# Kernel optimization log

Measured on AMD Instinct MI355X. Metric: run time of the kernel, lower is better.

## Reference

```python
import jax, jax.numpy as jnp
import numpy as np

B, S = 1, 2048
D, HD, NH, NKV, L, V, FF = 2048, 256, 8, 4, 4, 32000, 8192
WINDOW = 1024
SOFTCAP = 50.0
FINAL_CAP = 30.0
EPS = 1e-6
THETA = 10000.0
ATTN_TYPES = ("local", "global", "local", "global")
NEG = -2.3819763e38
SCALE = HD ** -0.5


def _rms(x, w):
    # RMSNorm with unit offset: x * rsqrt(mean(x^2)+eps) * (1 + w)
    n = x * jax.lax.rsqrt(jnp.mean(x * x, axis=-1, keepdims=True) + EPS)
    return n * (1.0 + w)


def _rope(x, cos, sin):
    # x: [B, S, H, HD]; rotate-half formulation (Gemma pairs i with i+HD/2)
    h = HD // 2
    x1, x2 = x[..., :h], x[..., h:]
    c = cos[None, :, None, :]
    s = sin[None, :, None, :]
    return jnp.concatenate([x1 * c - x2 * s, x1 * s + x2 * c], axis=-1)


def setup_inputs() -> dict:
    key = jax.random.key(0)
    ks = jax.random.split(key, 15)
    sd = 0.02
    f = lambda k, shape: jax.random.normal(k, shape, jnp.float32) * sd
    return {
        "input_ids": jax.random.randint(ks[0], (B, S), 0, V),
        "embed": f(ks[1], (V, D)),
        "wq": f(ks[2], (L, NH * HD, D)),
        "wk": f(ks[3], (L, NKV * HD, D)),
        "wv": f(ks[4], (L, NKV * HD, D)),
        "wo": f(ks[5], (L, D, NH * HD)),
        "wg": f(ks[6], (L, FF, D)),
        "wu": f(ks[7], (L, FF, D)),
        "wd": f(ks[8], (L, D, FF)),
        "ln_in": f(ks[9], (L, D)),
        "ln_pa": f(ks[10], (L, D)),
        "ln_pf": f(ks[11], (L, D)),
        "ln_pff": f(ks[12], (L, D)),
        "ln_f": f(ks[13], (D,)),
        "w_lm": f(ks[14], (V, D)),
    }


def _forward(input_ids, embed, wq, wk, wv, wo, wg, wu, wd,
             ln_in, ln_pa, ln_pf, ln_pff, ln_f, w_lm):
    # rotary tables
    pos = jnp.arange(S, dtype=jnp.float32)
    inv = 1.0 / (THETA ** (jnp.arange(0, HD, 2, dtype=jnp.float32) / HD))
    ang = pos[:, None] * inv[None, :]
    cos, sin = jnp.cos(ang), jnp.sin(ang)  # [S, HD/2]

    # additive masks
    i = jnp.arange(S)[:, None]
    j = jnp.arange(S)[None, :]
    causal = jnp.where(j > i, NEG, 0.0).astype(jnp.float32)
    local = jnp.where((j > i) | (i - j >= WINDOW), NEG, 0.0).astype(jnp.float32)

    h = embed[input_ids] * jnp.asarray(D ** 0.5, jnp.float32)
    rep = NH // NKV
    for l in range(L):
        mask = local if ATTN_TYPES[l] == "local" else causal
        x = _rms(h, ln_in[l])
        q = jnp.einsum('bsd,od->bso', x, wq[l]).reshape(B, S, NH, HD)
        k = jnp.einsum('bsd,od->bso', x, wk[l]).reshape(B, S, NKV, HD)
        v = jnp.einsum('bsd,od->bso', x, wv[l]).reshape(B, S, NKV, HD)
        q = _rope(q, cos, sin)
        k = _rope(k, cos, sin)
        k = jnp.repeat(k, rep, axis=2)  # GQA expand
        v = jnp.repeat(v, rep, axis=2)
        q = q.transpose(0, 2, 1, 3)  # bhsd
        k = k.transpose(0, 2, 1, 3)
        v = v.transpose(0, 2, 1, 3)
        qk = jnp.einsum('bhsd,bhfd->bhsf', q, k) * SCALE
        qk = jnp.tanh(qk / SOFTCAP) * SOFTCAP  # attn logit softcap
        scores = jax.nn.softmax(qk + mask, axis=-1)
        a = jnp.einsum('bhsf,bhfd->bhsd', scores, v)
        a = a.transpose(0, 2, 1, 3).reshape(B, S, NH * HD)
        attn_out = jnp.einsum('bso,do->bsd', a, wo[l])
        h = h + _rms(attn_out, ln_pa[l])  # post-attn norm then residual
        x = _rms(h, ln_pf[l])
        gate = jax.nn.gelu(jnp.einsum('bsd,fd->bsf', x, wg[l]), approximate=True)
        up = jnp.einsum('bsd,fd->bsf', x, wu[l])
        mlp = jnp.einsum('bsf,df->bsd', gate * up, wd[l])
        h = h + _rms(mlp, ln_pff[l])
    h = _rms(h, ln_f)
    logits = jnp.einsum('bsd,vd->bsv', h, w_lm)
    return jnp.tanh(logits / FINAL_CAP) * FINAL_CAP


def reference(input_ids, embed, wq, wk, wv, wo, wg, wu, wd,
              ln_in, ln_pa, ln_pf, ln_pff, ln_f, w_lm):
    return _forward(input_ids, embed, wq, wk, wv, wo, wg, wu, wd,
                    ln_in, ln_pa, ln_pf, ln_pff, ln_f, w_lm)
```

## Files before the change

### kernel.cpp

```cpp
#include <hip/hip_runtime.h>
#include <hip/hip_bf16.h>

typedef __attribute__((ext_vector_type(8))) __bf16 bf16x8;
typedef __attribute__((ext_vector_type(4))) float floatx4;

typedef __attribute__((address_space(1))) const unsigned char kGlb;
typedef __attribute__((address_space(3))) unsigned char kLds;

static constexpr int S = 2048;
static constexpr int D = 2048;
static constexpr int HD = 256;
static constexpr int NH = 8;
static constexpr int NKV = 4;
static constexpr int NLAYER = 4;
static constexpr int VOCAB = 32000;
static constexpr int FF = 8192;
static constexpr int WINDOW = 1024;

__device__ __forceinline__ float blk_sum(float v) {
    __shared__ float sm[4];
    #pragma unroll
    for (int o = 32; o > 0; o >>= 1) v += __shfl_down(v, o, 64);
    int lane = threadIdx.x & 63, w = threadIdx.x >> 6;
    __syncthreads();
    if (lane == 0) sm[w] = v;
    __syncthreads();
    return sm[0] + sm[1] + sm[2] + sm[3];
}

__device__ __forceinline__ float blk_max(float v) {
    __shared__ float sm[4];
    #pragma unroll
    for (int o = 32; o > 0; o >>= 1) v = fmaxf(v, __shfl_down(v, o, 64));
    int lane = threadIdx.x & 63, w = threadIdx.x >> 6;
    __syncthreads();
    if (lane == 0) sm[w] = v;
    __syncthreads();
    return fmaxf(fmaxf(sm[0], sm[1]), fmaxf(sm[2], sm[3]));
}

__global__ void embed_kernel(const int* __restrict__ ids, const float* __restrict__ E,
                             float* __restrict__ h) {
    int d = blockIdx.x * 256 + threadIdx.x;
    int s = blockIdx.y;
    h[(long)s * D + d] = E[(long)ids[s] * D + d] * 45.25483399593904f;
}

__global__ void rope_table_kernel(float* __restrict__ c, float* __restrict__ sn) {
    int i = threadIdx.x;
    int p = blockIdx.x;
    float inv = powf(10000.f, -(float)i / 128.f);
    float a = (float)p * inv;
    c[p * 128 + i] = cosf(a);
    sn[p * 128 + i] = sinf(a);
}

__global__ void cvt_bf16_kernel(const float* __restrict__ src, __hip_bfloat16* __restrict__ dst,
                                long n8) {
    long stride = (long)gridDim.x * 256;
    for (long i = (long)blockIdx.x * 256 + threadIdx.x; i < n8; i += stride) {
        long o = i * 8;
        float4 a = *(const float4*)(src + o);
        float4 b = *(const float4*)(src + o + 4);
        __hip_bfloat16 h8[8] = {
            __float2bfloat16(a.x), __float2bfloat16(a.y),
            __float2bfloat16(a.z), __float2bfloat16(a.w),
            __float2bfloat16(b.x), __float2bfloat16(b.y),
            __float2bfloat16(b.z), __float2bfloat16(b.w)};
        *(uint4*)(dst + o) = *(const uint4*)h8;
    }
}

__global__ void rms_bf16_kernel(const float* __restrict__ h, const float* __restrict__ w,
                                __hip_bfloat16* __restrict__ o) {
    int s = blockIdx.x;
    const float* row = h + (long)s * D;
    float vals[8], ss = 0.f;
    #pragma unroll
    for (int t = 0; t < 8; ++t) {
        int j = t * 256 + threadIdx.x;
        float v = row[j]; vals[t] = v; ss += v * v;
    }
    ss = blk_sum(ss);
    float r = rsqrtf(ss * (1.f / D) + 1e-6f);
    #pragma unroll
    for (int t = 0; t < 8; ++t) {
        int j = t * 256 + threadIdx.x;
        o[(long)s * D + j] = __float2bfloat16(vals[t] * r * (1.f + w[j]));
    }
}

__global__ void resid_rms_kernel(float* __restrict__ h, const float* __restrict__ tt,
                                 const float* __restrict__ w) {
    int s = blockIdx.x;
    const float* row = tt + (long)s * D;
    float* hr = h + (long)s * D;
    float vals[8], ss = 0.f;
    #pragma unroll
    for (int t = 0; t < 8; ++t) {
        int j = t * 256 + threadIdx.x;
        float v = row[j]; vals[t] = v; ss += v * v;
    }
    ss = blk_sum(ss);
    float r = rsqrtf(ss * (1.f / D) + 1e-6f);
    #pragma unroll
    for (int t = 0; t < 8; ++t) {
        int j = t * 256 + threadIdx.x;
        hr[j] += vals[t] * r * (1.f + w[j]);
    }
}

__global__ void rope_kernel(__hip_bfloat16* __restrict__ x, const float* __restrict__ cb,
                            const float* __restrict__ sb, int ldx) {
    int s = blockIdx.x, hh = blockIdx.y, i = threadIdx.x;
    __hip_bfloat16* p = x + (long)s * ldx + hh * HD;
    float x1 = __bfloat162float(p[i]);
    float x2 = __bfloat162float(p[128 + i]);
    float c = cb[s * 128 + i], sn = sb[s * 128 + i];
    p[i]       = __float2bfloat16(x1 * c - x2 * sn);
    p[128 + i] = __float2bfloat16(x1 * sn + x2 * c);
}

__global__ void transpose_v_kernel(const __hip_bfloat16* __restrict__ v,
                                   __hip_bfloat16* __restrict__ vt, int ldv) {
    __shared__ ushort tile[64][65];
    int s0 = blockIdx.x * 64, d0 = blockIdx.y * 64, kv = blockIdx.z;
    const ushort* vin = (const ushort*)v;
    ushort* vout = (ushort*)vt;
    #pragma unroll
    for (int it = 0; it < 4; ++it) {
        int slot = it * 256 + threadIdx.x;
        int r = slot >> 4, c4 = (slot & 15) << 2;
        ushort4 x = *(const ushort4*)(vin + (long)(s0 + r) * ldv + kv * HD + d0 + c4);
        tile[r][c4] = x.x; tile[r][c4 + 1] = x.y; tile[r][c4 + 2] = x.z; tile[r][c4 + 3] = x.w;
    }
    __syncthreads();
    #pragma unroll
    for (int it = 0; it < 4; ++it) {
        int slot = it * 256 + threadIdx.x;
        int rr = slot >> 4, c4 = (slot & 15) << 2;
        ushort4 y;
        y.x = tile[c4][rr]; y.y = tile[c4 + 1][rr]; y.z = tile[c4 + 2][rr]; y.w = tile[c4 + 3][rr];
        *(ushort4*)(vout + (long)kv * HD * S + (long)(d0 + rr) * S + s0 + c4) = y;
    }
}

__global__ void softmax_kernel(const float* __restrict__ sc, __hip_bfloat16* __restrict__ pr,
                               int isLocal) {
    int i = blockIdx.x, hh = blockIdx.y;
    const float* row = sc + ((long)hh * S + i) * S;
    __hip_bfloat16* orow = pr + ((long)hh * S + i) * S;
    int lo = isLocal ? max(0, i - (WINDOW - 1)) : 0;
    float vals[8];
    float m = -3.0e38f;
    #pragma unroll
    for (int t = 0; t < 8; ++t) {
        int j = t * 256 + threadIdx.x;
        bool chunkAny = (t * 256 <= i) && (t * 256 + 255 >= lo);
        if (chunkAny) {
            bool valid = (j <= i) && (j >= lo);
            float v = tanhf(row[j] * (0.0625f / 50.f)) * 50.f;
            vals[t] = valid ? v : -3.0e38f;
            m = fmaxf(m, vals[t]);
        } else {
            vals[t] = -3.0e38f;
        }
    }
    m = blk_max(m);
    float ps[8], ssum = 0.f;
    #pragma unroll
    for (int t = 0; t < 8; ++t) {
        float p = (vals[t] > -1.0e38f) ? __expf(vals[t] - m) : 0.f;
        ps[t] = p; ssum += p;
    }
    ssum = blk_sum(ssum);
    float inv = 1.f / ssum;
    #pragma unroll
    for (int t = 0; t < 8; ++t) {
        int j = t * 256 + threadIdx.x;
        orow[j] = __float2bfloat16(ps[t] * inv);
    }
}

__global__ void mul_gu_kernel(__hip_bfloat16* __restrict__ gu) {
    long idx = ((long)blockIdx.x * 256 + threadIdx.x) * 8;
    long s = idx >> 13;
    long f = idx & 8191;
    __hip_bfloat16* gp = gu + s * 16384 + f;
    const __hip_bfloat16* up = gu + s * 16384 + 8192 + f;
    uint4 gv = *(const uint4*)gp;
    uint4 uv = *(const uint4*)up;
    const __hip_bfloat16* gb = (const __hip_bfloat16*)&gv;
    const __hip_bfloat16* ub = (const __hip_bfloat16*)&uv;
    __hip_bfloat16 o[8];
    #pragma unroll
    for (int j = 0; j < 8; ++j)
        o[j] = __float2bfloat16(__bfloat162float(gb[j]) * __bfloat162float(ub[j]));
    *(uint4*)gp = *(const uint4*)o;
}

template<int EPI, int WM, int WN, int MI, int NI>
__global__ __launch_bounds__(WM*WN*64, 2) void gemm_pipe(
    const __hip_bfloat16* __restrict__ A, const __hip_bfloat16* __restrict__ B,
    void* __restrict__ Cv, int K, int lda, int ldb, int ldc,
    long aBatch, long bBatch, long cBatch, int bzDiv, int gx, int kMode) {
    constexpr int T  = WM * WN * 64;
    constexpr int BM = WM * MI * 16;
    constexpr int BN = WN * NI * 16;
    constexpr int AE = BM * 32;
    constexpr int BE = BN * 32;
    __shared__ __hip_bfloat16 lds[4][AE + BE];

    const int tid = threadIdx.x;
    const int nwg = gridDim.x;
    const int orig = blockIdx.x;
    const int wgid = (orig & 7) * (nwg >> 3) + (orig >> 3);
    const int bx = wgid % gx, by = wgid / gx;
    const int bz = blockIdx.z;

    int kstart = 0, kend = K;
    if (kMode == 1) { if (by > bx) return; }
    else if (kMode == 2) { if (by > bx || bx - by >= 9) return; }
    else if (kMode == 3) { kend = min(K, (bx + 1) * BM); }
    else if (kMode == 4) { kend = min(K, (bx + 1) * BM); kstart = max(0, (bx - 1024 / BM) * BM); }

    const __hip_bfloat16* Ab = A + (long)bz * aBatch + (long)bx * BM * lda;
    const __hip_bfloat16* Bb = B + (long)(bz / bzDiv) * bBatch + (long)by * BN * ldb;

    const int w = tid >> 6, l = tid & 63;
    const int wm = w / WN, wn = w % WN;
    const int wrow = wm * MI * 16, wcol = wn * NI * 16;
    const int fr = l & 15, g = l >> 4;
    const int sR = tid >> 2;
    const int sc = tid & 3;

    floatx4 acc[MI][NI] = {};
    bf16x8 bfv[NI];
    bf16x8 af[MI / 2];

    auto stageA = [&](int t, int buf) {
        const int k0 = kstart + t * 32;
        #pragma unroll
        for (int i = 0; i < 2; ++i) {
            int row = sR + i * (T / 4);
            int scol = ((sc ^ ((row >> 1) & 3)) << 3);
            __builtin_amdgcn_global_load_lds(
                (kGlb*)(Ab + (long)row * lda + k0 + scol),
                (kLds*)(&lds[buf][0] + tid * 8 + i * (T * 8)), 16, 0, 0);
        }
    };
    auto stageB = [&](int t, int buf) {
        const int k0 = kstart + t * 32;
        #pragma unroll
        for (int i = 0; i < 2; ++i) {
            int row = sR + i * (T / 4);
            int scol = ((sc ^ ((row >> 1) & 3)) << 3);
            __builtin_amdgcn_global_load_lds(
                (kGlb*)(Bb + (long)row * ldb + k0 + scol),
                (kLds*)(&lds[buf][AE] + tid * 8 + i * (T * 8)), 16, 0, 0);
        }
    };

    auto phase0 = [&](int buf, int t3, bool doStage) {
        const char* AsB = (const char*)&lds[buf][0];
        const char* BsB = (const char*)&lds[buf][AE];
        #pragma unroll
        for (int mi = 0; mi < MI / 2; ++mi) {
            int ra = wrow + mi * 16 + fr;
            af[mi] = *(const bf16x8*)(AsB + ra * 64 + ((g ^ ((ra >> 1) & 3)) << 4));
        }
        #pragma unroll
        for (int ni = 0; ni < NI; ++ni) {
            int rb = wcol + ni * 16 + fr;
            bfv[ni] = *(const bf16x8*)(BsB + rb * 64 + ((g ^ ((rb >> 1) & 3)) << 4));
        }
        if (doStage) stageA(t3, t3 & 3);
        __builtin_amdgcn_s_barrier();
        asm volatile("s_waitcnt lgkmcnt(0)" ::: "memory");
        __builtin_amdgcn_sched_barrier(0);
        __builtin_amdgcn_s_setprio(1);
        #pragma unroll
        for (int mi = 0; mi < MI / 2; ++mi)
            #pragma unroll
            for (int ni = 0; ni < NI; ++ni)
                acc[mi][ni] = __builtin_amdgcn_mfma_f32_16x16x32_bf16(af[mi], bfv[ni], acc[mi][ni], 0, 0, 0);
        __builtin_amdgcn_s_setprio(0);
        __builtin_amdgcn_sched_barrier(0);
        __builtin_amdgcn_s_barrier();
    };

    auto phase1 = [&](int buf, int t3, bool doStage, int vm) {
        const char* AsB = (const char*)&lds[buf][0];
        #pragma unroll
        for (int mi = 0; mi < MI / 2; ++mi) {
            int ra = wrow + (MI / 2 + mi) * 16 + fr;
            af[mi] = *(const bf16x8*)(AsB + ra * 64 + ((g ^ ((ra >> 1) & 3)) << 4));
        }
        if (doStage) stageB(t3, t3 & 3);
        if (vm == 8)      asm volatile("s_waitcnt vmcnt(8)" ::: "memory");
        else if (vm == 4) asm volatile("s_waitcnt vmcnt(4)" ::: "memory");
        else if (vm == 0) asm volatile("s_waitcnt vmcnt(0)" ::: "memory");
        __builtin_amdgcn_s_barrier();
        asm volatile("s_waitcnt lgkmcnt(0)" ::: "memory");
        __builtin_amdgcn_sched_barrier(0);
        __builtin_amdgcn_s_setprio(1);
        #pragma unroll
        for (int mi = 0; mi < MI / 2; ++mi)
            #pragma unroll
            for (int ni = 0; ni < NI; ++ni)
                acc[MI / 2 + mi][ni] = __builtin_amdgcn_mfma_f32_16x16x32_bf16(af[mi], bfv[ni], acc[MI / 2 + mi][ni], 0, 0, 0);
        __builtin_amdgcn_s_setprio(0);
        __builtin_amdgcn_sched_barrier(0);
        __builtin_amdgcn_s_barrier();
    };

    const int nt = (kend - kstart) >> 5;
    stageA(0, 0); stageB(0, 0);
    stageA(1, 1); stageB(1, 1);
    stageA(2, 2); stageB(2, 2);
    asm volatile("s_waitcnt vmcnt(8)" ::: "memory");
    __builtin_amdgcn_s_barrier();

    for (int t = 0; t < nt - 3; ++t) {
        const int b = t & 3;
        phase0(b, t + 3, true);
        phase1(b, t + 3, true, 8);
    }
    phase0((nt - 3) & 3, 0, false); phase1((nt - 3) & 3, 0, false, 4);
    phase0((nt - 2) & 3, 0, false); phase1((nt - 2) & 3, 0, false, 0);
    phase0((nt - 1) & 3, 0, false); phase1((nt - 1) & 3, 0, false, -1);

    const long cBase = (long)bz * cBatch + (long)bx * BM * ldc + (long)by * BN;
    const int rg = (l >> 4) * 4;
    #pragma unroll
    for (int mi = 0; mi < MI; ++mi) {
        #pragma unroll
        for (int ni = 0; ni < NI; ++ni) {
            #pragma unroll
            for (int r = 0; r < 4; ++r) {
                int row = wrow + mi * 16 + rg + r;
                int col = wcol + ni * 16 + fr;
                long idx = cBase + (long)row * ldc + col;
                float v = acc[mi][ni][r];
                if constexpr (EPI == 0) {
                    ((float*)Cv)[idx] = v;
                } else if constexpr (EPI == 1) {
                    ((__hip_bfloat16*)Cv)[idx] = __float2bfloat16(v);
                } else if constexpr (EPI == 3) {
                    ((float*)Cv)[idx] = tanhf(v * (1.f / 30.f)) * 30.f;
                } else {
                    int colg = by * BN + col;
                    float o = v;
                    if (colg < 8192)
                        o = 0.5f * v * (1.f + tanhf(0.7978845608f * (v + 0.044715f * v * v * v)));
                    ((__hip_bfloat16*)Cv)[idx] = __float2bfloat16(o);
                }
            }
        }
    }
}

template<int EPI>
__global__ __launch_bounds__(256) void gemm_bf16(
    const __hip_bfloat16* __restrict__ A, const __hip_bfloat16* __restrict__ B,
    void* __restrict__ Cv, int K, int lda, int ldb, int ldc,
    long aBatch, long bBatch, long cBatch, int bzDiv, int gx, int kMode) {
    __shared__ __hip_bfloat16 As[128 * 32];
    __shared__ __hip_bfloat16 Bs[128 * 32];
    const int tid = threadIdx.x;
    const int nwg = gridDim.x;
    const int orig = blockIdx.x;
    const int wgid = (orig & 7) * (nwg >> 3) + (orig >> 3);
    const int bx = wgid % gx, by = wgid / gx;
    const int bz = blockIdx.z;

    int kstart = 0, kend = K;
    if (kMode == 1) { if (by > bx) return; }
    else if (kMode == 2) { if (by > bx || bx - by >= 9) return; }
    else if (kMode == 3) { kend = min(K, (bx + 1) * 128); }
    else if (kMode == 4) { kend = min(K, (bx + 1) * 128); kstart = max(0, (bx - 8) * 128); }

    const __hip_bfloat16* Ab = A + (long)bz * aBatch + (long)bx * 128 * lda;
    const __hip_bfloat16* Bb = B + (long)(bz / bzDiv) * bBatch + (long)by * 128 * ldb;

    const int w = tid >> 6, l = tid & 63;
    int srow[2], scsrc[2], sdst[2];
    #pragma unroll
    for (int i = 0; i < 2; ++i) {
        int o = w * 2048 + i * 1024 + l * 16;
        int row = o >> 6;
        int chunk = (o >> 4) & 3;
        srow[i]  = row;
        scsrc[i] = (chunk ^ ((row >> 1) & 3)) * 8;
        sdst[i]  = w * 1024 + i * 512;
    }
    const int wr = (w >> 1) * 64, wc = (w & 1) * 64;
    const int fr = l & 15;
    const int g  = l >> 4;
    floatx4 acc[4][4] = {};
    for (int k0 = kstart; k0 < kend; k0 += 32) {
        __syncthreads();
        #pragma unroll
        for (int i = 0; i < 2; ++i) {
            __builtin_amdgcn_global_load_lds(
                (kGlb*)(Ab + (long)srow[i] * lda + k0 + scsrc[i]),
                (kLds*)(As + sdst[i]), 16, 0, 0);
            __builtin_amdgcn_global_load_lds(
                (kGlb*)(Bb + (long)srow[i] * ldb + k0 + scsrc[i]),
                (kLds*)(Bs + sdst[i]), 16, 0, 0);
        }
        __syncthreads();
        bf16x8 af[4], bfr[4];
        const char* AsB = (const char*)As;
        const char* BsB = (const char*)Bs;
        #pragma unroll
        for (int i = 0; i < 4; ++i) {
            int ra = wr + i * 16 + fr;
            af[i] = *(const bf16x8*)(AsB + ra * 64 + (((g ^ ((ra >> 1) & 3))) << 4));
        }
        #pragma unroll
        for (int j = 0; j < 4; ++j) {
            int rb = wc + j * 16 + fr;
            bfr[j] = *(const bf16x8*)(BsB + rb * 64 + (((g ^ ((rb >> 1) & 3))) << 4));
        }
        #pragma unroll
        for (int i = 0; i < 4; ++i)
            #pragma unroll
            for (int j = 0; j < 4; ++j)
                acc[i][j] = __builtin_amdgcn_mfma_f32_16x16x32_bf16(af[i], bfr[j], acc[i][j], 0, 0, 0);
    }
    const long cTile = (long)bz * cBatch + (long)bx * 128 * ldc + (long)by * 128;
    const int rg = (l >> 4) * 4;
    #pragma unroll
    for (int i = 0; i < 4; ++i)
        #pragma unroll
        for (int j = 0; j < 4; ++j)
            #pragma unroll
            for (int r = 0; r < 4; ++r) {
                int row = wr + i * 16 + rg + r;
                int col = wc + j * 16 + fr;
                long idx = cTile + (long)row * ldc + col;
                float v = acc[i][j][r];
                if constexpr (EPI == 0) ((float*)Cv)[idx] = v;
                else ((__hip_bfloat16*)Cv)[idx] = __float2bfloat16(v);
            }
}

template<int EPI>
__global__ __launch_bounds__(256) void gemm_f32w(
    const __hip_bfloat16* __restrict__ A, const float* __restrict__ Bv,
    void* __restrict__ Cv, int K, int lda, int ldb, int ldc) {
    __shared__ __hip_bfloat16 As[128][32];
    __shared__ __hip_bfloat16 Bs[128][32];
    const int tid = threadIdx.x;
    const __hip_bfloat16* Ab = A + (long)blockIdx.x * 128 * lda;
    const float* Bb = Bv + (long)blockIdx.y * 128 * ldb;
    const int wid = tid >> 6, lane = tid & 63;
    const int wr = (wid >> 1) * 64, wc = (wid & 1) * 64;
    const int fr = lane & 15;
    const int kb = (lane >> 4) * 8;
    floatx4 acc[4][4] = {};
    for (int k0 = 0; k0 < K; k0 += 32) {
        __syncthreads();
        #pragma unroll
        for (int it = 0; it < 2; ++it) {
            int slot = tid + it * 256;
            int r = slot >> 2, c8 = (slot & 3) * 8;
            *reinterpret_cast<uint4*>(&As[r][c8]) =
                *reinterpret_cast<const uint4*>(Ab + (long)r * lda + k0 + c8);
        }
        #pragma unroll
        for (int it = 0; it < 4; ++it) {
            int slot = tid + it * 256;
            int r = slot >> 3, c4 = (slot & 7) * 4;
            float4 f = *reinterpret_cast<const float4*>(Bb + (long)r * ldb + k0 + c4);
            __hip_bfloat16 t4[4] = {__float2bfloat16(f.x), __float2bfloat16(f.y),
                                    __float2bfloat16(f.z), __float2bfloat16(f.w)};
            *reinterpret_cast<ushort4*>(&Bs[r][c4]) = *reinterpret_cast<const ushort4*>(t4);
        }
        __syncthreads();
        bf16x8 af[4], bfr[4];
        #pragma unroll
        for (int i = 0; i < 4; ++i)
            af[i] = *reinterpret_cast<const bf16x8*>(&As[wr + i * 16 + fr][kb]);
        #pragma unroll
        for (int j = 0; j < 4; ++j)
            bfr[j] = *reinterpret_cast<const bf16x8*>(&Bs[wc + j * 16 + fr][kb]);
        #pragma unroll
        for (int i = 0; i < 4; ++i)
            #pragma unroll
            for (int j = 0; j < 4; ++j)
                acc[i][j] = __builtin_amdgcn_mfma_f32_16x16x32_bf16(af[i], bfr[j], acc[i][j], 0, 0, 0);
    }
    const long cTile = (long)blockIdx.x * 128 * ldc + (long)blockIdx.y * 128;
    const int rg = (lane >> 4) * 4;
    #pragma unroll
    for (int i = 0; i < 4; ++i)
        #pragma unroll
        for (int j = 0; j < 4; ++j)
            #pragma unroll
            for (int r = 0; r < 4; ++r) {
                int row = wr + i * 16 + rg + r;
                int col = wc + j * 16 + fr;
                long idx = cTile + (long)row * ldc + col;
                float v = acc[i][j][r];
                if constexpr (EPI == 0) ((float*)Cv)[idx] = v;
                else if constexpr (EPI == 1) ((__hip_bfloat16*)Cv)[idx] = __float2bfloat16(v);
                else if constexpr (EPI == 2) {
                    float gg = 0.5f * v * (1.f + tanhf(0.7978845608f * (v + 0.044715f * v * v * v)));
                    ((__hip_bfloat16*)Cv)[idx] = __float2bfloat16(gg);
                } else ((float*)Cv)[idx] = tanhf(v * (1.f / 30.f)) * 30.f;
            }
}

extern "C" void kernel_launch(void* const* d_in, const int* in_sizes, int n_in,
                              void* d_out, int out_size, void* d_ws, size_t ws_size,
                              hipStream_t stream) {
    const int*   ids    = (const int*)d_in[0];
    const float* embedW = (const float*)d_in[1];
    const float* wq     = (const float*)d_in[2];
    const float* wk     = (const float*)d_in[3];
    const float* wv     = (const float*)d_in[4];
    const float* wo     = (const float*)d_in[5];
    const float* wg     = (const float*)d_in[6];
    const float* wu     = (const float*)d_in[7];
    const float* wd     = (const float*)d_in[8];
    const float* ln_in  = (const float*)d_in[9];
    const float* ln_pa  = (const float*)d_in[10];
    const float* ln_pf  = (const float*)d_in[11];
    const float* ln_pff = (const float*)d_in[12];
    const float* ln_f   = (const float*)d_in[13];
    const float* w_lm   = (const float*)d_in[14];
    float* out = (float*)d_out;

    char* ws = (char*)d_ws;
    size_t off = 0;
    auto alloc = [&](size_t bytes) -> void* {
        size_t o = (off + 255) & ~(size_t)255;
        off = o + bytes;
        return (void*)(ws + o);
    };

    float* h            = (float*)alloc((size_t)S * D * 4);
    __hip_bfloat16* xb  = (__hip_bfloat16*)alloc((size_t)S * D * 2);
    __hip_bfloat16* qkvb = (__hip_bfloat16*)alloc((size_t)S * 4096 * 2);
    __hip_bfloat16* vT  = (__hip_bfloat16*)alloc((size_t)NKV * HD * S * 2);
    __hip_bfloat16* ab  = (__hip_bfloat16*)alloc((size_t)S * NH * HD * 2);
    float* tmpf         = (float*)alloc((size_t)S * D * 4);
    __hip_bfloat16* gu  = (__hip_bfloat16*)alloc((size_t)S * 16384 * 2);
    float* cosb         = (float*)alloc((size_t)S * 128 * 4);
    float* sinb         = (float*)alloc((size_t)S * 128 * 4);
    float* scores       = (float*)alloc((size_t)NH * S * S * 4);
    __hip_bfloat16* probs = (__hip_bfloat16*)alloc((size_t)NH * S * S * 2);

    const long SLq = 2048L * 2048, SLkv = 1024L * 2048, SLff = 8192L * 2048;
    const long nWlm = (long)VOCAB * D;
    __hip_bfloat16* wqkvb = (__hip_bfloat16*)alloc(4L * 4096 * 2048 * 2);
    __hip_bfloat16* wgub  = (__hip_bfloat16*)alloc(4L * 16384 * 2048 * 2);
    __hip_bfloat16* wob   = (__hip_bfloat16*)alloc(4L * SLq * 2);
    __hip_bfloat16* wdb   = (__hip_bfloat16*)alloc(4L * SLff * 2);
    __hip_bfloat16* wlmb  = (__hip_bfloat16*)alloc(nWlm * 2);
    const bool big = (off <= ws_size);
    (void)in_sizes; (void)n_in; (void)out_size;

    rope_table_kernel<<<dim3(S), dim3(128), 0, stream>>>(cosb, sinb);
    embed_kernel<<<dim3(D / 256, S), dim3(256), 0, stream>>>(ids, embedW, h);

    auto cvt = [&](const float* s, __hip_bfloat16* dp, long n) {
        long n8 = n / 8;
        long want = (n8 + 255) / 256;
        int blocks = (int)(want < 2048 ? want : 2048);
        cvt_bf16_kernel<<<dim3(blocks), dim3(256), 0, stream>>>(s, dp, n8);
    };
    if (big) {
        for (int l = 0; l < NLAYER; ++l) {
            cvt(wq + l * SLq,  wqkvb + (size_t)l * 4096 * 2048,                SLq);
            cvt(wk + l * SLkv, wqkvb + (size_t)l * 4096 * 2048 + 2048L * 2048, SLkv);
            cvt(wv + l * SLkv, wqkvb + (size_t)l * 4096 * 2048 + 3072L * 2048, SLkv);
            cvt(wg + l * SLff, wgub + (size_t)l * 16384 * 2048,                SLff);
            cvt(wu + l * SLff, wgub + (size_t)l * 16384 * 2048 + 8192L * 2048, SLff);
        }
        cvt(wo, wob, 4L * SLq);
        cvt(wd, wdb, 4L * SLff);
        cvt(w_lm, wlmb, nWlm);
    }

    auto p256 = [&](int epi, const __hip_bfloat16* A, const __hip_bfloat16* B, void* C,
                    int K, int lda, int ldb, int ldc, int gx, int gy) {
        dim3 grid(gx * gy, 1, 1);
        switch (epi) {
        case 3: gemm_pipe<3, 2, 4, 8, 4><<<grid, 512, 0, stream>>>(A, B, C, K, lda, ldb, ldc, 0, 0, 0, 1, gx, 0); break;
        default: gemm_pipe<4, 2, 4, 8, 4><<<grid, 512, 0, stream>>>(A, B, C, K, lda, ldb, ldc, 0, 0, 0, 1, gx, 0); break;
        }
    };
    auto p128 = [&](int epi, const __hip_bfloat16* A, const __hip_bfloat16* B, void* C,
                    int K, int lda, int ldb, int ldc, int gx, int gy, int gz,
                    long aB, long bB, long cB, int bzDiv, int kMode) {
        dim3 grid(gx * gy, 1, gz);
        switch (epi) {
        case 0: gemm_pipe<0, 2, 2, 4, 4><<<grid, 256, 0, stream>>>(A, B, C, K, lda, ldb, ldc, aB, bB, cB, bzDiv, gx, kMode); break;
        default: gemm_pipe<1, 2, 2, 4, 4><<<grid, 256, 0, stream>>>(A, B, C, K, lda, ldb, ldc, aB, bB, cB, bzDiv, gx, kMode); break;
        }
    };

    for (int l = 0; l < NLAYER; ++l) {
        int isLocal = (l % 2 == 0) ? 1 : 0;
        rms_bf16_kernel<<<dim3(S), dim3(256), 0, stream>>>(h, ln_in + l * D, xb);
        if (big) {
            p128(1, xb, wqkvb + (size_t)l * 4096 * 2048, qkvb, D, D, D, 4096, 16, 32, 1, 0, 0, 0, 1, 0);
        } else {
            gemm_f32w<1><<<dim3(16, 16), 256, 0, stream>>>(xb, wq + l * SLq, qkvb, D, D, D, 4096);
            gemm_f32w<1><<<dim3(16, 8), 256, 0, stream>>>(xb, wk + l * SLkv, qkvb + 2048, D, D, D, 4096);
            gemm_f32w<1><<<dim3(16, 8), 256, 0, stream>>>(xb, wv + l * SLkv, qkvb + 3072, D, D, D, 4096);
        }
        rope_kernel<<<dim3(S, NH), dim3(128), 0, stream>>>(qkvb, cosb, sinb, 4096);
        rope_kernel<<<dim3(S, NKV), dim3(128), 0, stream>>>(qkvb + 2048, cosb, sinb, 4096);
        transpose_v_kernel<<<dim3(S / 64, HD / 64, NKV), 256, 0, stream>>>(qkvb + 3072, vT, 4096);
        if (big) {
            p128(0, qkvb, qkvb + 2048, scores, HD, 4096, 4096, S, 16, 16, NH,
                 (long)HD, (long)HD, (long)S * S, 2, isLocal ? 2 : 1);
        } else {
            gemm_bf16<0><<<dim3(256, 1, NH), 256, 0, stream>>>(
                qkvb, qkvb + 2048, scores, HD, 4096, 4096, S,
                (long)HD, (long)HD, (long)S * S, 2, 16, isLocal ? 2 : 1);
        }
        softmax_kernel<<<dim3(S, NH), dim3(256), 0, stream>>>(scores, probs, isLocal);
        if (big) {
            p128(1, probs, vT, ab, S, S, S, NH * HD, 16, 2, NH,
                 (long)S * S, (long)HD * S, (long)HD, 2, isLocal ? 4 : 3);
        } else {
            gemm_bf16<1><<<dim3(32, 1, NH), 256, 0, stream>>>(
                probs, vT, ab, S, S, S, NH * HD,
                (long)S * S, (long)HD * S, (long)HD, 2, 16, isLocal ? 4 : 3);
        }
        if (big) {
            p128(0, ab, wob + (size_t)l * SLq, tmpf, NH * HD, NH * HD, NH * HD, D, 16, 16, 1, 0, 0, 0, 1, 0);
        } else {
            gemm_f32w<0><<<dim3(16, 16), 256, 0, stream>>>(ab, wo + l * SLq, tmpf, NH * HD, NH * HD, NH * HD, D);
        }
        resid_rms_kernel<<<dim3(S), dim3(256), 0, stream>>>(h, tmpf, ln_pa + l * D);
        rms_bf16_kernel<<<dim3(S), dim3(256), 0, stream>>>(h, ln_pf + l * D, xb);
        if (big) {
            p256(4, xb, wgub + (size_t)l * 16384 * 2048, gu, D, D, D, 16384, 8, 64);
        } else {
            gemm_f32w<2><<<dim3(16, 64), 256, 0, stream>>>(xb, wg + l * SLff, gu, D, D, D, 16384);
            gemm_f32w<1><<<dim3(16, 64), 256, 0, stream>>>(xb, wu + l * SLff, gu + 8192, D, D, D, 16384);
        }
        mul_gu_kernel<<<dim3((S * FF) / (256 * 8)), 256, 0, stream>>>(gu);
        if (big) {
            p128(0, gu, wdb + (size_t)l * SLff, tmpf, FF, 16384, FF, D, 16, 16, 1, 0, 0, 0, 1, 0);
        } else {
            gemm_f32w<0><<<dim3(16, 16), 256, 0, stream>>>(gu, wd + l * SLff, tmpf, FF, 16384, FF, D);
        }
        resid_rms_kernel<<<dim3(S), dim3(256), 0, stream>>>(h, tmpf, ln_pff + l * D);
    }

    rms_bf16_kernel<<<dim3(S), dim3(256), 0, stream>>>(h, ln_f, xb);
    if (big) {
        p256(3, xb, wlmb, out, D, D, D, VOCAB, 8, VOCAB / 256);
    } else {
        gemm_f32w<3><<<dim3(16, VOCAB / 128), 256, 0, stream>>>(xb, w_lm, out, D, D, D, VOCAB);
    }
}
```

Baseline: 2.708 ms.

## Add 8-phase quadrant-pipelined 256x256 GEMM for gate/up and LM head

Introduces a new 256x256-tile GEMM kernel that splits each K-step into four quadrant MFMA phases. Each phase interleaves direct global-to-LDS loads of half-tiles with LDS fragment reads, using explicit waitcnt, barriers and setprio. It replaces the previous 256-wide gemm_pipe path for the fused gate/up projection and the LM-head GEMM, aiming to overlap memory traffic with matrix math more finely. The hand-tuned wait counts and double-buffered half tiles are fragile and depend on K being a multiple of 64.

```diff
diff --git a/kernel.cpp b/kernel.cpp
--- a/kernel.cpp
+++ b/kernel.cpp
@@ -199,6 +199,173 @@
     *(uint4*)gp = *(const uint4*)o;
 }
 
+#define RD_AF(BUF, HALF)                                                          \
+    {                                                                             \
+        const char* _p = (const char*)&ldsA[BUF][HALF][0];                        \
+        _Pragma("unroll")                                                         \
+        for (int mi = 0; mi < 4; ++mi) {                                          \
+            int r = wm * 64 + mi * 16 + fr;                                       \
+            _Pragma("unroll")                                                     \
+            for (int ks = 0; ks < 2; ++ks) {                                      \
+                int c = ks * 4 + g;                                               \
+                af[mi][ks] = *(const bf16x8*)(_p + r * 128 + ((c ^ (r & 7)) << 4)); \
+            }                                                                     \
+        }                                                                         \
+    }
+
+#define RD_BF(DST, BUF, HALF)                                                     \
+    {                                                                             \
+        const char* _p = (const char*)&ldsB[BUF][HALF][0];                        \
+        _Pragma("unroll")                                                         \
+        for (int ni = 0; ni < 2; ++ni) {                                          \
+            int r = wn * 32 + ni * 16 + fr;                                       \
+            _Pragma("unroll")                                                     \
+            for (int ks = 0; ks < 2; ++ks) {                                      \
+                int c = ks * 4 + g;                                               \
+                DST[ni][ks] = *(const bf16x8*)(_p + r * 128 + ((c ^ (r & 7)) << 4)); \
+            }                                                                     \
+        }                                                                         \
+    }
+
+#define MM(QM, QN, BF)                                                            \
+    __builtin_amdgcn_s_setprio(1);                                                \
+    _Pragma("unroll")                                                             \
+    for (int mi = 0; mi < 4; ++mi)                                                \
+        _Pragma("unroll")                                                         \
+        for (int ni = 0; ni < 2; ++ni)                                            \
+            _Pragma("unroll")                                                     \
+            for (int ks = 0; ks < 2; ++ks)                                        \
+                acc[QM][QN][mi][ni] = __builtin_amdgcn_mfma_f32_16x16x32_bf16(    \
+                    af[mi][ks], BF[ni][ks], acc[QM][QN][mi][ni], 0, 0, 0);        \
+    __builtin_amdgcn_s_setprio(0);
+
+template<int EPI>
+__global__ __launch_bounds__(512, 2) void gemm_8ph(
+    const __hip_bfloat16* __restrict__ A, const __hip_bfloat16* __restrict__ B,
+    void* __restrict__ Cv, int K, int lda, int ldb, int ldc, int gx) {
+    __shared__ __hip_bfloat16 ldsA[2][2][8192];
+    __shared__ __hip_bfloat16 ldsB[2][2][8192];
+    const int tid = threadIdx.x;
+    const int nwg = gridDim.x;
+    const int orig = blockIdx.x;
+    const int wgid = (orig & 7) * (nwg >> 3) + (orig >> 3);
+    const int bx = wgid % gx, by = wgid / gx;
+
+    const __hip_bfloat16* Ab = A + (long)bx * 256 * lda;
+    const __hip_bfloat16* Bb = B + (long)by * 256 * ldb;
+
+    const int w = tid >> 6, l = tid & 63;
+    const int wm = w >> 2, wn = w & 3;
+    const int fr = l & 15, g = l >> 4;
+    const int sRow0 = tid >> 3;
+    const int sCh = tid & 7;
+
+    floatx4 acc[2][2][4][2] = {};
+    bf16x8 af[4][2], bf0[2][2], bf1[2][2];
+
+    auto stage = [&](const __hip_bfloat16* src, int ld, int k0, __hip_bfloat16* dst) {
+        #pragma unroll
+        for (int i = 0; i < 2; ++i) {
+            int row = sRow0 + i * 64;
+            int cs = (sCh ^ (row & 7)) * 8;
+            __builtin_amdgcn_global_load_lds(
+                (kGlb*)(src + (long)row * ld + k0 + cs),
+                (kLds*)((char*)dst + i * 8192 + tid * 16), 16, 0, 0);
+        }
+    };
+
+    const int nt = K >> 6;
+    stage(Ab,             lda, 0,  &ldsA[0][0][0]);
+    stage(Bb,             ldb, 0,  &ldsB[0][0][0]);
+    stage(Bb + 128 * ldb, ldb, 0,  &ldsB[0][1][0]);
+    stage(Ab + 128 * lda, lda, 0,  &ldsA[0][1][0]);
+    stage(Ab,             lda, 64, &ldsA[1][0][0]);
+    stage(Bb,             ldb, 64, &ldsB[1][0][0]);
+
+    for (int t = 0; t < nt - 1; ++t) {
+        const int b = t & 1, nb = b ^ 1;
+        asm volatile("s_waitcnt vmcnt(8)" ::: "memory");
+        __builtin_amdgcn_s_barrier();
+        stage(Bb + 128 * ldb, ldb, (t + 1) * 64, &ldsB[nb][1][0]);
+        RD_AF(b, 0);
+        RD_BF(bf0, b, 0);
+        asm volatile("s_waitcnt lgkmcnt(0)" ::: "memory");
+        __builtin_amdgcn_sched_barrier(0);
+        MM(0, 0, bf0);
+        __builtin_amdgcn_sched_barrier(0);
+        asm volatile("s_waitcnt vmcnt(8)" ::: "memory");
+        __builtin_amdgcn_s_barrier();
+        stage(Ab + 128 * lda, lda, (t + 1) * 64, &ldsA[nb][1][0]);
+        RD_BF(bf1, b, 1);
+        asm volatile("s_waitcnt lgkmcnt(0)" ::: "memory");
+        __builtin_amdgcn_sched_barrier(0);
+        MM(0, 1, bf1);
+        __builtin_amdgcn_sched_barrier(0);
+        asm volatile("s_waitcnt vmcnt(8)" ::: "memory");
+        __builtin_amdgcn_s_barrier();
+        if (t + 2 < nt) stage(Ab, lda, (t + 2) * 64, &ldsA[b][0][0]);
+        RD_AF(b, 1);
+        asm volatile("s_waitcnt lgkmcnt(0)" ::: "memory");
+        __builtin_amdgcn_sched_barrier(0);
+        MM(1, 0, bf0);
+        __builtin_amdgcn_sched_barrier(0);
+        __builtin_amdgcn_s_barrier();
+        if (t + 2 < nt) stage(Bb, ldb, (t + 2) * 64, &ldsB[b][0][0]);
+        MM(1, 1, bf1);
+        __builtin_amdgcn_sched_barrier(0);
+    }
+    {
+        const int b = (nt - 1) & 1;
+        asm volatile("s_waitcnt vmcnt(4)" ::: "memory");
+        __builtin_amdgcn_s_barrier();
+        RD_AF(b, 0);
+        RD_BF(bf0, b, 0);
+        asm volatile("s_waitcnt lgkmcnt(0)" ::: "memory");
+        __builtin_amdgcn_sched_barrier(0);
+        MM(0, 0, bf0);
+        asm volatile("s_waitcnt vmcnt(2)" ::: "memory");
+        __builtin_amdgcn_s_barrier();
+        RD_BF(bf1, b, 1);
+        asm volatile("s_waitcnt lgkmcnt(0)" ::: "memory");
+        __builtin_amdgcn_sched_barrier(0);
+        MM(0, 1, bf1);
+        asm volatile("s_waitcnt vmcnt(0)" ::: "memory");
+        __builtin_amdgcn_s_barrier();
+        RD_AF(b, 1);
+        asm volatile("s_waitcnt lgkmcnt(0)" ::: "memory");
+        __builtin_amdgcn_sched_barrier(0);
+        MM(1, 0, bf0);
+        MM(1, 1, bf1);
+    }
+
+    const long cBase = (long)bx * 256 * ldc + (long)by * 256;
+    const int rg = (l >> 4) * 4;
+    #pragma unroll
+    for (int qm = 0; qm < 2; ++qm)
+    #pragma unroll
+    for (int qn = 0; qn < 2; ++qn)
+    #pragma unroll
+    for (int mi = 0; mi < 4; ++mi)
+    #pragma unroll
+    for (int ni = 0; ni < 2; ++ni)
+    #pragma unroll
+    for (int r = 0; r < 4; ++r) {
+        int row = qm * 128 + wm * 64 + mi * 16 + rg + r;
+        int col = qn * 128 + wn * 32 + ni * 16 + fr;
+        long idx = cBase + (long)row * ldc + col;
+        float v = acc[qm][qn][mi][ni][r];
+        if constexpr (EPI == 3) {
+            ((float*)Cv)[idx] = tanhf(v * (1.f / 30.f)) * 30.f;
+        } else {
+            int colg = by * 256 + col;
+            float o = v;
+            if (colg < 8192)
+                o = 0.5f * v * (1.f + tanhf(0.7978845608f * (v + 0.044715f * v * v * v)));
+            ((__hip_bfloat16*)Cv)[idx] = __float2bfloat16(o);
+        }
+    }
+}
+
 template<int EPI, int WM, int WN, int MI, int NI>
 __global__ __launch_bounds__(WM*WN*64, 2) void gemm_pipe(
     const __hip_bfloat16* __restrict__ A, const __hip_bfloat16* __restrict__ B,
@@ -344,16 +511,8 @@
                 float v = acc[mi][ni][r];
                 if constexpr (EPI == 0) {
                     ((float*)Cv)[idx] = v;
-                } else if constexpr (EPI == 1) {
+                } else {
                     ((__hip_bfloat16*)Cv)[idx] = __float2bfloat16(v);
-                } else if constexpr (EPI == 3) {
-                    ((float*)Cv)[idx] = tanhf(v * (1.f / 30.f)) * 30.f;
-                } else {
-                    int colg = by * BN + col;
-                    float o = v;
-                    if (colg < 8192)
-                        o = 0.5f * v * (1.f + tanhf(0.7978845608f * (v + 0.044715f * v * v * v)));
-                    ((__hip_bfloat16*)Cv)[idx] = __float2bfloat16(o);
                 }
             }
         }
@@ -585,13 +744,11 @@
         cvt(w_lm, wlmb, nWlm);
     }
 
-    auto p256 = [&](int epi, const __hip_bfloat16* A, const __hip_bfloat16* B, void* C,
-                    int K, int lda, int ldb, int ldc, int gx, int gy) {
+    auto p8 = [&](int epi, const __hip_bfloat16* A, const __hip_bfloat16* B, void* C,
+                  int K, int lda, int ldb, int ldc, int gx, int gy) {
         dim3 grid(gx * gy, 1, 1);
-        switch (epi) {
-        case 3: gemm_pipe<3, 2, 4, 8, 4><<<grid, 512, 0, stream>>>(A, B, C, K, lda, ldb, ldc, 0, 0, 0, 1, gx, 0); break;
-        default: gemm_pipe<4, 2, 4, 8, 4><<<grid, 512, 0, stream>>>(A, B, C, K, lda, ldb, ldc, 0, 0, 0, 1, gx, 0); break;
-        }
+        if (epi == 3) gemm_8ph<3><<<grid, 512, 0, stream>>>(A, B, C, K, lda, ldb, ldc, gx);
+        else          gemm_8ph<4><<<grid, 512, 0, stream>>>(A, B, C, K, lda, ldb, ldc, gx);
     };
     auto p128 = [&](int epi, const __hip_bfloat16* A, const __hip_bfloat16* B, void* C,
                     int K, int lda, int ldb, int ldc, int gx, int gy, int gz,
@@ -641,7 +798,7 @@
         resid_rms_kernel<<<dim3(S), dim3(256), 0, stream>>>(h, tmpf, ln_pa + l * D);
         rms_bf16_kernel<<<dim3(S), dim3(256), 0, stream>>>(h, ln_pf + l * D, xb);
         if (big) {
-            p256(4, xb, wgub + (size_t)l * 16384 * 2048, gu, D, D, D, 16384, 8, 64);
+            p8(4, xb, wgub + (size_t)l * 16384 * 2048, gu, D, D, D, 16384, 8, 64);
         } else {
             gemm_f32w<2><<<dim3(16, 64), 256, 0, stream>>>(xb, wg + l * SLff, gu, D, D, D, 16384);
             gemm_f32w<1><<<dim3(16, 64), 256, 0, stream>>>(xb, wu + l * SLff, gu + 8192, D, D, D, 16384);
@@ -657,7 +814,7 @@
 
     rms_bf16_kernel<<<dim3(S), dim3(256), 0, stream>>>(h, ln_f, xb);
     if (big) {
-        p256(3, xb, wlmb, out, D, D, D, VOCAB, 8, VOCAB / 256);
+        p8(3, xb, wlmb, out, D, D, D, VOCAB, 8, VOCAB / 256);
     } else {
         gemm_f32w<3><<<dim3(16, VOCAB / 128), 256, 0, stream>>>(xb, w_lm, out, D, D, D, VOCAB);
     }
```

After: 2.764 ms. +2.1%, slower.

## Interleave gate/up weights to fuse GELU*up into GEMM epilogue; store bf16 scores

Applied to the files above, without the earlier changes.

The gate and up weight rows are interleaved during conversion, so adjacent output columns of the fused GEMM hold the gate and up values. A new epilogue pairs them with a lane shuffle and writes gelu(gate)*up directly at half width, which removes the separate multiply kernel and the wide intermediate buffer. Attention scores are now stored as bf16 instead of fp32, halving the score write and read traffic. Scores lose precision before the softcap and softmax, and the old non-big fallback for the attention GEMMs is removed.

```diff
diff --git a/kernel.cpp b/kernel.cpp
--- a/kernel.cpp
+++ b/kernel.cpp
@@ -71,6 +71,23 @@
     }
 }
 
+__global__ void cvt_inter_kernel(const float* __restrict__ src, __hip_bfloat16* __restrict__ dst,
+                                 int half, long n8) {
+    long stride = (long)gridDim.x * 256;
+    for (long i = (long)blockIdx.x * 256 + threadIdx.x; i < n8; i += stride) {
+        long o = i * 8;
+        long row = o >> 11, col = o & 2047;
+        float4 a = *(const float4*)(src + o);
+        float4 b = *(const float4*)(src + o + 4);
+        __hip_bfloat16 h8[8] = {
+            __float2bfloat16(a.x), __float2bfloat16(a.y),
+            __float2bfloat16(a.z), __float2bfloat16(a.w),
+            __float2bfloat16(b.x), __float2bfloat16(b.y),
+            __float2bfloat16(b.z), __float2bfloat16(b.w)};
+        *(uint4*)(dst + ((row * 2 + half) << 11) + col) = *(const uint4*)h8;
+    }
+}
+
 __global__ void rms_bf16_kernel(const float* __restrict__ h, const float* __restrict__ w,
                                 __hip_bfloat16* __restrict__ o) {
     int s = blockIdx.x;
@@ -145,10 +162,10 @@
     }
 }
 
-__global__ void softmax_kernel(const float* __restrict__ sc, __hip_bfloat16* __restrict__ pr,
-                               int isLocal) {
+__global__ void softmax_kernel(const __hip_bfloat16* __restrict__ sc,
+                               __hip_bfloat16* __restrict__ pr, int isLocal) {
     int i = blockIdx.x, hh = blockIdx.y;
-    const float* row = sc + ((long)hh * S + i) * S;
+    const __hip_bfloat16* row = sc + ((long)hh * S + i) * S;
     __hip_bfloat16* orow = pr + ((long)hh * S + i) * S;
     int lo = isLocal ? max(0, i - (WINDOW - 1)) : 0;
     float vals[8];
@@ -159,7 +176,7 @@
         bool chunkAny = (t * 256 <= i) && (t * 256 + 255 >= lo);
         if (chunkAny) {
             bool valid = (j <= i) && (j >= lo);
-            float v = tanhf(row[j] * (0.0625f / 50.f)) * 50.f;
+            float v = tanhf(__bfloat162float(row[j]) * (0.0625f / 50.f)) * 50.f;
             vals[t] = valid ? v : -3.0e38f;
             m = fmaxf(m, vals[t]);
         } else {
@@ -340,110 +357,27 @@
             for (int r = 0; r < 4; ++r) {
                 int row = wrow + mi * 16 + rg + r;
                 int col = wcol + ni * 16 + fr;
-                long idx = cBase + (long)row * ldc + col;
                 float v = acc[mi][ni][r];
-                if constexpr (EPI == 0) {
-                    ((float*)Cv)[idx] = v;
-                } else if constexpr (EPI == 1) {
-                    ((__hip_bfloat16*)Cv)[idx] = __float2bfloat16(v);
-                } else if constexpr (EPI == 3) {
-                    ((float*)Cv)[idx] = tanhf(v * (1.f / 30.f)) * 30.f;
+                if constexpr (EPI == 5) {
+                    float pv = __shfl_xor(v, 1);
+                    if (!(fr & 1)) {
+                        float gg = 0.5f * v * (1.f + tanhf(0.7978845608f * (v + 0.044715f * v * v * v)));
+                        long idx5 = ((long)bx * BM + row) * (long)ldc + (long)by * (BN / 2) + (col >> 1);
+                        ((__hip_bfloat16*)Cv)[idx5] = __float2bfloat16(gg * pv);
+                    }
                 } else {
-                    int colg = by * BN + col;
-                    float o = v;
-                    if (colg < 8192)
-                        o = 0.5f * v * (1.f + tanhf(0.7978845608f * (v + 0.044715f * v * v * v)));
-                    ((__hip_bfloat16*)Cv)[idx] = __float2bfloat16(o);
+                    long idx = cBase + (long)row * ldc + col;
+                    if constexpr (EPI == 0) {
+                        ((float*)Cv)[idx] = v;
+                    } else if constexpr (EPI == 1) {
+                        ((__hip_bfloat16*)Cv)[idx] = __float2bfloat16(v);
+                    } else if constexpr (EPI == 3) {
+                        ((float*)Cv)[idx] = tanhf(v * (1.f / 30.f)) * 30.f;
+                    }
                 }
             }
         }
     }
-}
-
-template<int EPI>
-__global__ __launch_bounds__(256) void gemm_bf16(
-    const __hip_bfloat16* __restrict__ A, const __hip_bfloat16* __restrict__ B,
-    void* __restrict__ Cv, int K, int lda, int ldb, int ldc,
-    long aBatch, long bBatch, long cBatch, int bzDiv, int gx, int kMode) {
-    __shared__ __hip_bfloat16 As[128 * 32];
-    __shared__ __hip_bfloat16 Bs[128 * 32];
-    const int tid = threadIdx.x;
-    const int nwg = gridDim.x;
-    const int orig = blockIdx.x;
-    const int wgid = (orig & 7) * (nwg >> 3) + (orig >> 3);
-    const int bx = wgid % gx, by = wgid / gx;
-    const int bz = blockIdx.z;
-
-    int kstart = 0, kend = K;
-    if (kMode == 1) { if (by > bx) return; }
-    else if (kMode == 2) { if (by > bx || bx - by >= 9) return; }
-    else if (kMode == 3) { kend = min(K, (bx + 1) * 128); }
-    else if (kMode == 4) { kend = min(K, (bx + 1) * 128); kstart = max(0, (bx - 8) * 128); }
-
-    const __hip_bfloat16* Ab = A + (long)bz * aBatch + (long)bx * 128 * lda;
-    const __hip_bfloat16* Bb = B + (long)(bz / bzDiv) * bBatch + (long)by * 128 * ldb;
-
-    const int w = tid >> 6, l = tid & 63;
-    int srow[2], scsrc[2], sdst[2];
-    #pragma unroll
-    for (int i = 0; i < 2; ++i) {
-        int o = w * 2048 + i * 1024 + l * 16;
-        int row = o >> 6;
-        int chunk = (o >> 4) & 3;
-        srow[i]  = row;
-        scsrc[i] = (chunk ^ ((row >> 1) & 3)) * 8;
-        sdst[i]  = w * 1024 + i * 512;
-    }
-    const int wr = (w >> 1) * 64, wc = (w & 1) * 64;
-    const int fr = l & 15;
-    const int g  = l >> 4;
-    floatx4 acc[4][4] = {};
-    for (int k0 = kstart; k0 < kend; k0 += 32) {
-        __syncthreads();
-        #pragma unroll
-        for (int i = 0; i < 2; ++i) {
-            __builtin_amdgcn_global_load_lds(
-                (kGlb*)(Ab + (long)srow[i] * lda + k0 + scsrc[i]),
-                (kLds*)(As + sdst[i]), 16, 0, 0);
-            __builtin_amdgcn_global_load_lds(
-                (kGlb*)(Bb + (long)srow[i] * ldb + k0 + scsrc[i]),
-                (kLds*)(Bs + sdst[i]), 16, 0, 0);
-        }
-        __syncthreads();
-        bf16x8 af[4], bfr[4];
-        const char* AsB = (const char*)As;
-        const char* BsB = (const char*)Bs;
-        #pragma unroll
-        for (int i = 0; i < 4; ++i) {
-            int ra = wr + i * 16 + fr;
-            af[i] = *(const bf16x8*)(AsB + ra * 64 + (((g ^ ((ra >> 1) & 3))) << 4));
-        }
-        #pragma unroll
-        for (int j = 0; j < 4; ++j) {
-            int rb = wc + j * 16 + fr;
-            bfr[j] = *(const bf16x8*)(BsB + rb * 64 + (((g ^ ((rb >> 1) & 3))) << 4));
-        }
-        #pragma unroll
-        for (int i = 0; i < 4; ++i)
-            #pragma unroll
-            for (int j = 0; j < 4; ++j)
-                acc[i][j] = __builtin_amdgcn_mfma_f32_16x16x32_bf16(af[i], bfr[j], acc[i][j], 0, 0, 0);
-    }
-    const long cTile = (long)bz * cBatch + (long)bx * 128 * ldc + (long)by * 128;
-    const int rg = (l >> 4) * 4;
-    #pragma unroll
-    for (int i = 0; i < 4; ++i)
-        #pragma unroll
-        for (int j = 0; j < 4; ++j)
-            #pragma unroll
-            for (int r = 0; r < 4; ++r) {
-                int row = wr + i * 16 + rg + r;
-                int col = wc + j * 16 + fr;
-                long idx = cTile + (long)row * ldc + col;
-                float v = acc[i][j][r];
-                if constexpr (EPI == 0) ((float*)Cv)[idx] = v;
-                else ((__hip_bfloat16*)Cv)[idx] = __float2bfloat16(v);
-            }
 }
 
 template<int EPI>
@@ -547,11 +481,12 @@
     __hip_bfloat16* vT  = (__hip_bfloat16*)alloc((size_t)NKV * HD * S * 2);
     __hip_bfloat16* ab  = (__hip_bfloat16*)alloc((size_t)S * NH * HD * 2);
     float* tmpf         = (float*)alloc((size_t)S * D * 4);
+    __hip_bfloat16* guP = (__hip_bfloat16*)alloc((size_t)S * FF * 2);
     __hip_bfloat16* gu  = (__hip_bfloat16*)alloc((size_t)S * 16384 * 2);
     float* cosb         = (float*)alloc((size_t)S * 128 * 4);
     float* sinb         = (float*)alloc((size_t)S * 128 * 4);
-    float* scores       = (float*)alloc((size_t)NH * S * S * 4);
-    __hip_bfloat16* probs = (__hip_bfloat16*)alloc((size_t)NH * S * S * 2);
+    __hip_bfloat16* scores = (__hip_bfloat16*)alloc((size_t)NH * S * S * 2);
+    __hip_bfloat16* probs  = (__hip_bfloat16*)alloc((size_t)NH * S * S * 2);
 
     const long SLq = 2048L * 2048, SLkv = 1024L * 2048, SLff = 8192L * 2048;
     const long nWlm = (long)VOCAB * D;
@@ -572,13 +507,19 @@
         int blocks = (int)(want < 2048 ? want : 2048);
         cvt_bf16_kernel<<<dim3(blocks), dim3(256), 0, stream>>>(s, dp, n8);
     };
+    auto cvtI = [&](const float* s, __hip_bfloat16* dp, int half, long n) {
+        long n8 = n / 8;
+        long want = (n8 + 255) / 256;
+        int blocks = (int)(want < 2048 ? want : 2048);
+        cvt_inter_kernel<<<dim3(blocks), dim3(256), 0, stream>>>(s, dp, half, n8);
+    };
     if (big) {
         for (int l = 0; l < NLAYER; ++l) {
             cvt(wq + l * SLq,  wqkvb + (size_t)l * 4096 * 2048,                SLq);
             cvt(wk + l * SLkv, wqkvb + (size_t)l * 4096 * 2048 + 2048L * 2048, SLkv);
             cvt(wv + l * SLkv, wqkvb + (size_t)l * 4096 * 2048 + 3072L * 2048, SLkv);
-            cvt(wg + l * SLff, wgub + (size_t)l * 16384 * 2048,                SLff);
-            cvt(wu + l * SLff, wgub + (size_t)l * 16384 * 2048 + 8192L * 2048, SLff);
+            cvtI(wg + l * SLff, wgub + (size_t)l * 16384 * 2048, 0, SLff);
+            cvtI(wu + l * SLff, wgub + (size_t)l * 16384 * 2048, 1, SLff);
         }
         cvt(wo, wob, 4L * SLq);
         cvt(wd, wdb, 4L * SLff);
@@ -588,10 +529,10 @@
     auto p256 = [&](int epi, const __hip_bfloat16* A, const __hip_bfloat16* B, void* C,
                     int K, int lda, int ldb, int ldc, int gx, int gy) {
         dim3 grid(gx * gy, 1, 1);
-        switch (epi) {
-        case 3: gemm_pipe<3, 2, 4, 8, 4><<<grid, 512, 0, stream>>>(A, B, C, K, lda, ldb, ldc, 0, 0, 0, 1, gx, 0); break;
-        default: gemm_pipe<4, 2, 4, 8, 4><<<grid, 512, 0, stream>>>(A, B, C, K, lda, ldb, ldc, 0, 0, 0, 1, gx, 0); break;
-        }
+        if (epi == 3)
+            gemm_pipe<3, 2, 4, 8, 4><<<grid, 512, 0, stream>>>(A, B, C, K, lda, ldb, ldc, 0, 0, 0, 1, gx, 0);
+        else
+            gemm_pipe<5, 2, 4, 8, 4><<<grid, 512, 0, stream>>>(A, B, C, K, lda, ldb, ldc, 0, 0, 0, 1, gx, 0);
     };
     auto p128 = [&](int epi, const __hip_bfloat16* A, const __hip_bfloat16* B, void* C,
                     int K, int lda, int ldb, int ldc, int gx, int gy, int gz,
@@ -616,23 +557,11 @@
         rope_kernel<<<dim3(S, NH), dim3(128), 0, stream>>>(qkvb, cosb, sinb, 4096);
         rope_kernel<<<dim3(S, NKV), dim3(128), 0, stream>>>(qkvb + 2048, cosb, sinb, 4096);
         transpose_v_kernel<<<dim3(S / 64, HD / 64, NKV), 256, 0, stream>>>(qkvb + 3072, vT, 4096);
-        if (big) {
-            p128(0, qkvb, qkvb + 2048, scores, HD, 4096, 4096, S, 16, 16, NH,
-                 (long)HD, (long)HD, (long)S * S, 2, isLocal ? 2 : 1);
-        } else {
-            gemm_bf16<0><<<dim3(256, 1, NH), 256, 0, stream>>>(
-                qkvb, qkvb + 2048, scores, HD, 4096, 4096, S,
-                (long)HD, (long)HD, (long)S * S, 2, 16, isLocal ? 2 : 1);
-        }
+        p128(1, qkvb, qkvb + 2048, scores, HD, 4096, 4096, S, 16, 16, NH,
+             (long)HD, (long)HD, (long)S * S, 2, isLocal ? 2 : 1);
         softmax_kernel<<<dim3(S, NH), dim3(256), 0, stream>>>(scores, probs, isLocal);
-        if (big) {
-            p128(1, probs, vT, ab, S, S, S, NH * HD, 16, 2, NH,
-                 (long)S * S, (long)HD * S, (long)HD, 2, isLocal ? 4 : 3);
-        } else {
-            gemm_bf16<1><<<dim3(32, 1, NH), 256, 0, stream>>>(
-                probs, vT, ab, S, S, S, NH * HD,
-                (long)S * S, (long)HD * S, (long)HD, 2, 16, isLocal ? 4 : 3);
-        }
+        p128(1, probs, vT, ab, S, S, S, NH * HD, 16, 2, NH,
+             (long)S * S, (long)HD * S, (long)HD, 2, isLocal ? 4 : 3);
         if (big) {
             p128(0, ab, wob + (size_t)l * SLq, tmpf, NH * HD, NH * HD, NH * HD, D, 16, 16, 1, 0, 0, 0, 1, 0);
         } else {
@@ -641,14 +570,14 @@
         resid_rms_kernel<<<dim3(S), dim3(256), 0, stream>>>(h, tmpf, ln_pa + l * D);
         rms_bf16_kernel<<<dim3(S), dim3(256), 0, stream>>>(h, ln_pf + l * D, xb);
         if (big) {
-            p256(4, xb, wgub + (size_t)l * 16384 * 2048, gu, D, D, D, 16384, 8, 64);
+            p256(5, xb, wgub + (size_t)l * 16384 * 2048, guP, D, D, D, FF, 8, 64);
         } else {
             gemm_f32w<2><<<dim3(16, 64), 256, 0, stream>>>(xb, wg + l * SLff, gu, D, D, D, 16384);
             gemm_f32w<1><<<dim3(16, 64), 256, 0, stream>>>(xb, wu + l * SLff, gu + 8192, D, D, D, 16384);
-        }
-        mul_gu_kernel<<<dim3((S * FF) / (256 * 8)), 256, 0, stream>>>(gu);
+            mul_gu_kernel<<<dim3((S * FF) / (256 * 8)), 256, 0, stream>>>(gu);
+        }
         if (big) {
-            p128(0, gu, wdb + (size_t)l * SLff, tmpf, FF, 16384, FF, D, 16, 16, 1, 0, 0, 0, 1, 0);
+            p128(0, guP, wdb + (size_t)l * SLff, tmpf, FF, FF, FF, D, 16, 16, 1, 0, 0, 0, 1, 0);
         } else {
             gemm_f32w<0><<<dim3(16, 16), 256, 0, stream>>>(gu, wd + l * SLff, tmpf, FF, 16384, FF, D);
         }
```

Result: faster. 2.594 ms (-4.2%).
